# Optimization experiments

Measured on AMD Instinct MI355X. Metric: run time of the kernel, lower is better.

The kernel has to match this reference:

```python
import jax, jax.numpy as jnp
import numpy as np

HEADS = 16

def setup_inputs() -> dict:
    key = jax.random.key(0)
    k1, k2, k3 = jax.random.split(key, 3)
    B, S, D = 2, 2048, 1024
    return {
        "query": jax.random.normal(k1, (B, S, D), dtype=jnp.float32),
        "key": jax.random.normal(k2, (B, S, D), dtype=jnp.float32),
        "value": jax.random.normal(k3, (B, S, D), dtype=jnp.float32),
    }

def reference(query, key, value):
    B, S, D = query.shape
    H = HEADS
    dh = D // H
    # split(-1) into H equal chunks == reshape to (B, S, H, dh)
    q = query.reshape(B, S, H, dh)
    k = key.reshape(B, S, H, dh)
    v = value.reshape(B, S, H, dh)
    scale = 1.0 / jnp.sqrt(jnp.asarray(dh, dtype=query.dtype))
    scores = jnp.einsum('bqhd,bkhd->bhqk', q, k) * scale  # [B,H,S,S]
    probs = jax.nn.softmax(scores, axis=-1)
    out = jnp.einsum('bhqk,bkhd->bqhd', probs, v)  # [B,S,H,dh]
    return out.reshape(B, S, D)
```

## Files before the change

kernel.cpp:

```cpp
#include <hip/hip_runtime.h>
#include <stdint.h>


#define B_ 2
#define S_ 2048
#define D_ 1024
#define H_ 16
#define DH 64
#define M_TILE 128
#define N_TILE 128
#define NITER (S_ / N_TILE)

typedef __bf16 bf16;
typedef __bf16 bf16x2 __attribute__((ext_vector_type(2)));
typedef __bf16 bf16x4 __attribute__((ext_vector_type(4)));
typedef __bf16 bf16x8 __attribute__((ext_vector_type(8)));
typedef float floatx4 __attribute__((ext_vector_type(4)));

#define KB_HEAD (S_ * DH * 2)
#define KB_TOTAL (B_ * H_ * KB_HEAD)
#define VT_ROW (S_ * 2)
#define WS_NEEDED (2u * KB_TOTAL)

#define KTILE_B 16384
#define BUF_B 32768
#define LSH_OFF 65536
#define SMEM_MAIN (LSH_OFF + 512)
#define O_STRIDE 36

__device__ __forceinline__ float fast_exp2(float x) {
#if __has_builtin(__builtin_amdgcn_exp2f)
  return __builtin_amdgcn_exp2f(x);
#else
  return exp2f(x);
#endif
}

__device__ __forceinline__ void gl_lds16(const void* g, void* l) {
  __builtin_amdgcn_global_load_lds(
      (const __attribute__((address_space(1))) unsigned int*)g,
      (__attribute__((address_space(3))) unsigned int*)l, 16, 0, 0);
}

__global__ __launch_bounds__(256)
void prep(const float* __restrict__ Kg, const float* __restrict__ Vg,
          unsigned char* __restrict__ ws) {
  const int bid = blockIdx.x;
  const int tid = threadIdx.x;
  if (bid < 512) {
    __shared__ __align__(16) bf16 VTsh[64][132];
    const int head_lin = bid & 31, ktile = bid >> 5;
    const int b = head_lin >> 4, h = head_lin & 15;
    const int kb = ktile * 128;
    const int vr0 = (tid >> 3) << 2;
    const int vf0 = (tid & 7) << 3;
    const float* Vbase = Vg + (size_t)(b * S_) * D_ + h * DH;
    float vals[4][8];
#pragma unroll
    for (int rr = 0; rr < 4; ++rr) {
      const float* vp = Vbase + (size_t)(kb + vr0 + rr) * D_ + vf0;
      float4 a = *(const float4*)vp;
      float4 c = *(const float4*)(vp + 4);
      vals[rr][0] = a.x; vals[rr][1] = a.y; vals[rr][2] = a.z; vals[rr][3] = a.w;
      vals[rr][4] = c.x; vals[rr][5] = c.y; vals[rr][6] = c.z; vals[rr][7] = c.w;
    }
    const int pbase = (vr0 & 96) + ((vr0 >> 2) & 3) * 8 + ((vr0 >> 4) & 1) * 4;
#pragma unroll
    for (int j = 0; j < 8; ++j) {
      bf16x4 y = {(bf16)vals[0][j], (bf16)vals[1][j], (bf16)vals[2][j], (bf16)vals[3][j]};
      *(bf16x4*)(&VTsh[vf0 + j][pbase]) = y;
    }
    __syncthreads();
    const int f = tid >> 2, part = tid & 3;
    unsigned char* dst = ws + KB_TOTAL + (size_t)(head_lin * 64 + f) * VT_ROW + kb * 2 + part * 64;
#pragma unroll
    for (int c16 = 0; c16 < 4; ++c16) {
      bf16x8 v = *(const bf16x8*)(&VTsh[f][part * 32 + c16 * 8]);
      *(bf16x8*)(dst + c16 * 16) = v;
    }
  } else {
    const int cb = bid - 512;
#pragma unroll
    for (int i = 0; i < 8; ++i) {
      int idx = cb * 2048 + i * 256 + tid;
      int f4 = idx & 15;
      int hh = (idx >> 4) & 15;
      int s  = (idx >> 8) & 2047;
      int bb = idx >> 19;
      float4 x = *(const float4*)(Kg + (size_t)idx * 4);
      bf16x4 y = {(bf16)x.x, (bf16)x.y, (bf16)x.z, (bf16)x.w};
      *(bf16x4*)(ws + (size_t)(((bb * 16 + hh) * 2048 + s) * 16 + f4) * 8) = y;
    }
  }
}

__global__ __launch_bounds__(512, 4)
void attn_fwd(const float* __restrict__ Qg, const unsigned char* __restrict__ Kb,
              const unsigned char* __restrict__ VT, float* __restrict__ Og) {
  __shared__ __align__(16) unsigned char smem[SMEM_MAIN];
  float* Osh = (float*)smem;
  float* Lsh = (float*)(smem + LSH_OFF);

  const int tid  = threadIdx.x;
  const int lane = tid & 63;
  const int wave = tid >> 6;
  const int kw   = wave & 1;
  const int qw   = wave >> 1;
  const int col  = lane & 15;
  const int quad = lane >> 4;

  const int bid      = blockIdx.x;
  const int head_lin = bid & 31;
  const int qtile    = bid >> 5;
  const int b        = head_lin >> 4;
  const int h        = head_lin & 15;

  const unsigned char* Khead = Kb + (size_t)head_lin * KB_HEAD;
  const unsigned char* Vhead = VT + (size_t)head_lin * (DH * VT_ROW);

  const float QSCALE = 0.125f * 1.44269504088896340736f;

  bf16x8 Qf[2][2];
#pragma unroll
  for (int qt = 0; qt < 2; ++qt) {
    const float* base = Qg + (size_t)(b * S_ + qtile * M_TILE + qw * 32 + qt * 16 + col) * D_
                        + h * DH + quad * 8;
#pragma unroll
    for (int ks = 0; ks < 2; ++ks) {
      float4 x0 = *(const float4*)(base + ks * 32);
      float4 x1 = *(const float4*)(base + ks * 32 + 4);
      bf16x8 f;
      f[0] = (bf16)(x0.x * QSCALE); f[1] = (bf16)(x0.y * QSCALE);
      f[2] = (bf16)(x0.z * QSCALE); f[3] = (bf16)(x0.w * QSCALE);
      f[4] = (bf16)(x1.x * QSCALE); f[5] = (bf16)(x1.y * QSCALE);
      f[6] = (bf16)(x1.z * QSCALE); f[7] = (bf16)(x1.w * QSCALE);
      Qf[qt][ks] = f;
    }
  }

  floatx4 accO[4][2];
  float l_lane[2] = {0.f, 0.f};
#pragma unroll
  for (int ft = 0; ft < 4; ++ft)
#pragma unroll
    for (int qt = 0; qt < 2; ++qt) accO[ft][qt] = (floatx4)0.f;

  const int krow_b = wave * 16 + (lane >> 3);
  const int kcg    = lane & 7;
  const int vf_b   = wave * 8 + (lane >> 4);
  const int vcg    = lane & 15;

  const int krow0   = kw * 64 + col;
  const int ka0_off = krow0 * 128 + ((quad ^ (col & 7)) << 4);
  const int ka1_off = krow0 * 128 + (((quad | 4) ^ (col & 7)) << 4);
  const int va_c0   = KTILE_B + col * 256 + ((((kw << 3) | quad) ^ col) << 4);
  const int va_c1   = KTILE_B + col * 256 + ((((kw << 3) | 4 | quad) ^ col) << 4);

  auto dma_tile = [&](int kbk, int bufoff) {
#pragma unroll
    for (int t = 0; t < 2; ++t) {
      const int r = krow_b + t * 8;
      gl_lds16(Khead + (size_t)(kbk + r) * 128 + ((kcg ^ (r & 7)) << 4),
               smem + bufoff + (wave * 16 + t * 8) * 128);
    }
#pragma unroll
    for (int t = 0; t < 2; ++t) {
      const int f = vf_b + t * 4;
      gl_lds16(Vhead + (size_t)f * VT_ROW + kbk * 2 + ((vcg ^ (f & 15)) << 4),
               smem + bufoff + KTILE_B + (wave * 8 + t * 4) * 256);
    }
  };

  dma_tile(0, 0);
  __syncthreads();

  for (int it = 0; it < NITER; ++it) {
    const int bc = (it & 1) << 15;
    if (it + 1 < NITER) dma_tile((it + 1) * N_TILE, bc ^ BUF_B);

    floatx4 accS[4][2];
#pragma unroll
    for (int kt = 0; kt < 4; ++kt) {
      bf16x8 Ka0 = *(const bf16x8*)(smem + bc + ka0_off + kt * 2048);
      bf16x8 Ka1 = *(const bf16x8*)(smem + bc + ka1_off + kt * 2048);
#pragma unroll
      for (int qt = 0; qt < 2; ++qt) {
        floatx4 a = (floatx4)0.f;
        a = __builtin_amdgcn_mfma_f32_16x16x32_bf16(Ka0, Qf[qt][0], a, 0, 0, 0);
        a = __builtin_amdgcn_mfma_f32_16x16x32_bf16(Ka1, Qf[qt][1], a, 0, 0, 0);
        accS[kt][qt] = a;
      }
    }

#pragma unroll
    for (int qt = 0; qt < 2; ++qt) {
      float rs = 0.f;
#pragma unroll
      for (int kt = 0; kt < 4; ++kt)
#pragma unroll
        for (int r = 0; r < 4; ++r) {
          float p = fast_exp2(accS[kt][qt][r]);
          accS[kt][qt][r] = p;
          rs += p;
        }
      l_lane[qt] += rs;
    }

#pragma unroll
    for (int c = 0; c < 2; ++c) {
      bf16x8 Pf[2];
#pragma unroll
      for (int qt = 0; qt < 2; ++qt) {
        floatx4 p0 = accS[2 * c][qt], p1 = accS[2 * c + 1][qt];
        bf16x8 f = {(bf16)p0[0], (bf16)p0[1], (bf16)p0[2], (bf16)p0[3],
                    (bf16)p1[0], (bf16)p1[1], (bf16)p1[2], (bf16)p1[3]};
        Pf[qt] = f;
      }
      const int vo = c ? va_c1 : va_c0;
#pragma unroll
      for (int ft = 0; ft < 4; ++ft) {
        bf16x8 Va = *(const bf16x8*)(smem + bc + vo + ft * 4096);
#pragma unroll
        for (int qt = 0; qt < 2; ++qt)
          accO[ft][qt] = __builtin_amdgcn_mfma_f32_16x16x32_bf16(Va, Pf[qt], accO[ft][qt], 0, 0, 0);
      }
    }
    __syncthreads();
  }

  float l_red[2];
#pragma unroll
  for (int qt = 0; qt < 2; ++qt) {
    float s = l_lane[qt];
    s += __shfl_xor(s, 16);
    s += __shfl_xor(s, 32);
    l_red[qt] = s;
  }

  if (kw == 1) {
    float* r = Osh + (qw * 64 + lane) * O_STRIDE;
#pragma unroll
    for (int qt = 0; qt < 2; ++qt)
#pragma unroll
      for (int ft = 0; ft < 4; ++ft)
        *(floatx4*)(r + (qt * 4 + ft) * 4) = accO[ft][qt];
    if (quad == 0) {
#pragma unroll
      for (int qt = 0; qt < 2; ++qt)
        Lsh[qw * 32 + qt * 16 + col] = l_red[qt];
    }
  }
  __syncthreads();

  if (kw == 0) {
    const float* r = Osh + (qw * 64 + lane) * O_STRIDE;
    float rl[2];
#pragma unroll
    for (int qt = 0; qt < 2; ++qt)
      rl[qt] = 1.0f / (l_red[qt] + Lsh[qw * 32 + qt * 16 + col]);
#pragma unroll
    for (int qt = 0; qt < 2; ++qt) {
      const int q = qtile * M_TILE + qw * 32 + qt * 16 + col;
      float* dst = Og + (size_t)(b * S_ + q) * D_ + h * DH + quad * 4;
#pragma unroll
      for (int ft = 0; ft < 4; ++ft) {
        floatx4 o = (accO[ft][qt] + *(const floatx4*)(r + (qt * 4 + ft) * 4)) * rl[qt];
        *(floatx4*)(dst + ft * 16) = o;
      }
    }
  }
}

#define FB_K_STRIDE 68
#define FB_V_STRIDE 132
#define FB_K_BYTES (128 * FB_K_STRIDE * 2)
#define FB_V_BYTES (64 * FB_V_STRIDE * 2)
#define FB_ML_OFF (FB_K_BYTES + FB_V_BYTES)
#define FB_SMEM (FB_ML_OFF + 2048)

__device__ __forceinline__ bf16x8 cat8(bf16x4 a, bf16x4 b) {
  return __builtin_shufflevector(a, b, 0, 1, 2, 3, 4, 5, 6, 7);
}

__global__ __launch_bounds__(512, 4)
void attn_fwd_fb(const float* __restrict__ Qg, const float* __restrict__ Kg,
                 const float* __restrict__ Vg, float* __restrict__ Og) {
  __shared__ __align__(16) unsigned char smem[FB_SMEM > (256 * O_STRIDE * 4 + 2048) ? FB_SMEM : (256 * O_STRIDE * 4 + 2048)];
  bf16*  Ksh = (bf16*)smem;
  bf16*  Vsh = (bf16*)(smem + FB_K_BYTES);
  float* Osh = (float*)smem;
  float* Lsh = (float*)(smem + 256 * O_STRIDE * 4);

  const int tid  = threadIdx.x;
  const int lane = tid & 63;
  const int wave = tid >> 6;
  const int kw   = wave & 1;
  const int qw   = wave >> 1;
  const int col  = lane & 15;
  const int quad = lane >> 4;
  const int bid      = blockIdx.x;
  const int head_lin = bid & 31;
  const int qtile    = bid >> 5;
  const int b        = head_lin >> 4;
  const int h        = head_lin & 15;
  const float QSCALE = 0.125f * 1.44269504088896340736f;

  bf16x8 Qf[2][2];
#pragma unroll
  for (int qt = 0; qt < 2; ++qt) {
    const float* base = Qg + (size_t)(b * S_ + qtile * M_TILE + qw * 32 + qt * 16 + col) * D_
                        + h * DH + quad * 8;
#pragma unroll
    for (int ks = 0; ks < 2; ++ks) {
      float4 x0 = *(const float4*)(base + ks * 32);
      float4 x1 = *(const float4*)(base + ks * 32 + 4);
      bf16x8 f;
      f[0] = (bf16)(x0.x * QSCALE); f[1] = (bf16)(x0.y * QSCALE);
      f[2] = (bf16)(x0.z * QSCALE); f[3] = (bf16)(x0.w * QSCALE);
      f[4] = (bf16)(x1.x * QSCALE); f[5] = (bf16)(x1.y * QSCALE);
      f[6] = (bf16)(x1.z * QSCALE); f[7] = (bf16)(x1.w * QSCALE);
      Qf[qt][ks] = f;
    }
  }

  floatx4 accO[4][2];
  float l_lane[2] = {0.f, 0.f};
#pragma unroll
  for (int ft = 0; ft < 4; ++ft)
#pragma unroll
    for (int qt = 0; qt < 2; ++qt) accO[ft][qt] = (floatx4)0.f;

  const float* Kbase = Kg + (size_t)(b * S_) * D_ + h * DH;
  const float* Vbase = Vg + (size_t)(b * S_) * D_ + h * DH;
  const int krow0 = tid >> 4;
  const int kf4   = tid & 15;
  const int vk0   = (tid >> 3) * 2;
  const int vf0   = (tid & 7) * 8;

  for (int it = 0; it < NITER; ++it) {
    const int kb = it * N_TILE;
    float4 kx[4];
#pragma unroll
    for (int i = 0; i < 4; ++i)
      kx[i] = *(const float4*)(Kbase + (size_t)(kb + krow0 + 32 * i) * D_ + kf4 * 4);
    float4 va0 = *(const float4*)(Vbase + (size_t)(kb + vk0) * D_ + vf0);
    float4 va1 = *(const float4*)(Vbase + (size_t)(kb + vk0) * D_ + vf0 + 4);
    float4 vb0 = *(const float4*)(Vbase + (size_t)(kb + vk0 + 1) * D_ + vf0);
    float4 vb1 = *(const float4*)(Vbase + (size_t)(kb + vk0 + 1) * D_ + vf0 + 4);
#pragma unroll
    for (int i = 0; i < 4; ++i) {
      bf16x4 y = {(bf16)kx[i].x, (bf16)kx[i].y, (bf16)kx[i].z, (bf16)kx[i].w};
      *(bf16x4*)(Ksh + (krow0 + 32 * i) * FB_K_STRIDE + kf4 * 4) = y;
    }
    {
      float a[8] = {va0.x, va0.y, va0.z, va0.w, va1.x, va1.y, va1.z, va1.w};
      float c[8] = {vb0.x, vb0.y, vb0.z, vb0.w, vb1.x, vb1.y, vb1.z, vb1.w};
#pragma unroll
      for (int j = 0; j < 8; ++j) {
        bf16x2 y = {(bf16)a[j], (bf16)c[j]};
        *(bf16x2*)(Vsh + (vf0 + j) * FB_V_STRIDE + vk0) = y;
      }
    }
    __syncthreads();

    floatx4 accS[4][2];
#pragma unroll
    for (int kt = 0; kt < 4; ++kt) {
      const bf16* kp = Ksh + (kw * 64 + kt * 16 + col) * FB_K_STRIDE + quad * 8;
      bf16x8 Ka0 = cat8(*(const bf16x4*)kp, *(const bf16x4*)(kp + 4));
      bf16x8 Ka1 = cat8(*(const bf16x4*)(kp + 32), *(const bf16x4*)(kp + 36));
#pragma unroll
      for (int qt = 0; qt < 2; ++qt) {
        floatx4 a = (floatx4)0.f;
        a = __builtin_amdgcn_mfma_f32_16x16x32_bf16(Ka0, Qf[qt][0], a, 0, 0, 0);
        a = __builtin_amdgcn_mfma_f32_16x16x32_bf16(Ka1, Qf[qt][1], a, 0, 0, 0);
        accS[kt][qt] = a;
      }
    }
#pragma unroll
    for (int qt = 0; qt < 2; ++qt) {
      float rs = 0.f;
#pragma unroll
      for (int kt = 0; kt < 4; ++kt)
#pragma unroll
        for (int r = 0; r < 4; ++r) {
          float p = fast_exp2(accS[kt][qt][r]);
          accS[kt][qt][r] = p;
          rs += p;
        }
      l_lane[qt] += rs;
    }
#pragma unroll
    for (int c = 0; c < 2; ++c) {
      bf16x8 Pf[2];
#pragma unroll
      for (int qt = 0; qt < 2; ++qt) {
        floatx4 p0 = accS[2 * c][qt], p1 = accS[2 * c + 1][qt];
        bf16x8 f = {(bf16)p0[0], (bf16)p0[1], (bf16)p0[2], (bf16)p0[3],
                    (bf16)p1[0], (bf16)p1[1], (bf16)p1[2], (bf16)p1[3]};
        Pf[qt] = f;
      }
#pragma unroll
      for (int ft = 0; ft < 4; ++ft) {
        const bf16* vp = Vsh + (ft * 16 + col) * FB_V_STRIDE + kw * 64 + 32 * c + quad * 4;
        bf16x8 Va = cat8(*(const bf16x4*)vp, *(const bf16x4*)(vp + 16));
#pragma unroll
        for (int qt = 0; qt < 2; ++qt)
          accO[ft][qt] = __builtin_amdgcn_mfma_f32_16x16x32_bf16(Va, Pf[qt], accO[ft][qt], 0, 0, 0);
      }
    }
    __syncthreads();
  }

  float l_red[2];
#pragma unroll
  for (int qt = 0; qt < 2; ++qt) {
    float s = l_lane[qt];
    s += __shfl_xor(s, 16);
    s += __shfl_xor(s, 32);
    l_red[qt] = s;
  }
  if (kw == 1) {
    float* r = Osh + (qw * 64 + lane) * O_STRIDE;
#pragma unroll
    for (int qt = 0; qt < 2; ++qt)
#pragma unroll
      for (int ft = 0; ft < 4; ++ft)
        *(floatx4*)(r + (qt * 4 + ft) * 4) = accO[ft][qt];
    if (quad == 0) {
#pragma unroll
      for (int qt = 0; qt < 2; ++qt)
        Lsh[qw * 32 + qt * 16 + col] = l_red[qt];
    }
  }
  __syncthreads();
  if (kw == 0) {
    const float* r = Osh + (qw * 64 + lane) * O_STRIDE;
    float rl[2];
#pragma unroll
    for (int qt = 0; qt < 2; ++qt)
      rl[qt] = 1.0f / (l_red[qt] + Lsh[qw * 32 + qt * 16 + col]);
#pragma unroll
    for (int qt = 0; qt < 2; ++qt) {
      const int q = qtile * M_TILE + qw * 32 + qt * 16 + col;
      float* dst = Og + (size_t)(b * S_ + q) * D_ + h * DH + quad * 4;
#pragma unroll
      for (int ft = 0; ft < 4; ++ft) {
        floatx4 o = (accO[ft][qt] + *(const floatx4*)(r + (qt * 4 + ft) * 4)) * rl[qt];
        *(floatx4*)(dst + ft * 16) = o;
      }
    }
  }
}

extern "C" void kernel_launch(void* const* d_in, const int* in_sizes, int n_in,
                              void* d_out, int out_size, void* d_ws, size_t ws_size,
                              hipStream_t stream) {
  const float* Q = (const float*)d_in[0];
  const float* K = (const float*)d_in[1];
  const float* V = (const float*)d_in[2];
  float* O = (float*)d_out;
  if (ws_size >= WS_NEEDED && d_ws != nullptr) {
    unsigned char* ws = (unsigned char*)d_ws;
    hipLaunchKernelGGL(prep, dim3(1024), dim3(256), 0, stream, K, V, ws);
    hipLaunchKernelGGL(attn_fwd, dim3(B_ * H_ * (S_ / M_TILE)), dim3(512), 0, stream,
                       Q, ws, ws + KB_TOTAL, O);
  } else {
    hipLaunchKernelGGL(attn_fwd_fb, dim3(B_ * H_ * (S_ / M_TILE)), dim3(512), 0, stream,
                       Q, K, V, O);
  }
}
```

Baseline: 129.9 us.

## Halve attention tiles to 64x64, stagger KV start per block, vectorize K prep

Cuts the main attention kernel's query and key tiles from 128 to 64 and its block size from 512 to 256 threads, doubling the grid to 1024 blocks, and shrinks the shared-memory buffers so more blocks can reside per CU. Each block now begins its key/value sweep at an offset set by its query tile, so concurrent blocks read different KV tiles instead of all hitting the same one. The K conversion in prep is rewritten to use 8-wide bf16 stores in a head-major order and runs more blocks. The fallback kernel is changed to keep its 128 tiling. In exchange, K/V tiles are reused across fewer queries, so total KV traffic from L2 doubles and per-block sync overhead grows.

```diff
diff --git a/kernel.cpp b/kernel.cpp
--- a/kernel.cpp
+++ b/kernel.cpp
@@ -7,8 +7,8 @@
 #define D_ 1024
 #define H_ 16
 #define DH 64
-#define M_TILE 128
-#define N_TILE 128
+#define M_TILE 64
+#define N_TILE 64
 #define NITER (S_ / N_TILE)
 
 typedef __bf16 bf16;
@@ -22,9 +22,9 @@
 #define VT_ROW (S_ * 2)
 #define WS_NEEDED (2u * KB_TOTAL)
 
-#define KTILE_B 16384
-#define BUF_B 32768
-#define LSH_OFF 65536
+#define KTILE_B 8192
+#define BUF_B 16384
+#define LSH_OFF 32768
 #define SMEM_MAIN (LSH_OFF + 512)
 #define O_STRIDE 36
 
@@ -81,20 +81,23 @@
   } else {
     const int cb = bid - 512;
 #pragma unroll
-    for (int i = 0; i < 8; ++i) {
-      int idx = cb * 2048 + i * 256 + tid;
-      int f4 = idx & 15;
-      int hh = (idx >> 4) & 15;
-      int s  = (idx >> 8) & 2047;
-      int bb = idx >> 19;
-      float4 x = *(const float4*)(Kg + (size_t)idx * 4);
-      bf16x4 y = {(bf16)x.x, (bf16)x.y, (bf16)x.z, (bf16)x.w};
-      *(bf16x4*)(ws + (size_t)(((bb * 16 + hh) * 2048 + s) * 16 + f4) * 8) = y;
-    }
-  }
-}
-
-__global__ __launch_bounds__(512, 4)
+    for (int i = 0; i < 2; ++i) {
+      int idx = cb * 512 + i * 256 + tid;
+      int f8 = idx & 7;
+      int s  = (idx >> 3) & 2047;
+      int hh = (idx >> 14) & 15;
+      int bb = idx >> 18;
+      const float* src = Kg + (size_t)(bb * 2048 + s) * 1024 + hh * 64 + f8 * 8;
+      float4 x0 = ((const float4*)src)[0];
+      float4 x1 = ((const float4*)src)[1];
+      bf16x8 y = {(bf16)x0.x, (bf16)x0.y, (bf16)x0.z, (bf16)x0.w,
+                  (bf16)x1.x, (bf16)x1.y, (bf16)x1.z, (bf16)x1.w};
+      *(bf16x8*)(ws + (size_t)idx * 16) = y;
+    }
+  }
+}
+
+__global__ __launch_bounds__(256, 4)
 void attn_fwd(const float* __restrict__ Qg, const unsigned char* __restrict__ Kb,
               const unsigned char* __restrict__ VT, float* __restrict__ Og) {
   __shared__ __align__(16) unsigned char smem[SMEM_MAIN];
@@ -145,42 +148,40 @@
 #pragma unroll
     for (int qt = 0; qt < 2; ++qt) accO[ft][qt] = (floatx4)0.f;
 
-  const int krow_b = wave * 16 + (lane >> 3);
-  const int kcg    = lane & 7;
-  const int vf_b   = wave * 8 + (lane >> 4);
-  const int vcg    = lane & 15;
-
-  const int krow0   = kw * 64 + col;
-  const int ka0_off = krow0 * 128 + ((quad ^ (col & 7)) << 4);
-  const int ka1_off = krow0 * 128 + (((quad | 4) ^ (col & 7)) << 4);
-  const int va_c0   = KTILE_B + col * 256 + ((((kw << 3) | quad) ^ col) << 4);
-  const int va_c1   = KTILE_B + col * 256 + ((((kw << 3) | 4 | quad) ^ col) << 4);
+  const int dr = lane >> 3;
+  const int dc = (lane & 7) ^ dr;
+  const int c7      = col & 7;
+  const int ka0_off = (kw * 32 + col) * 128 + ((quad ^ c7) << 4);
+  const int ka1_off = (kw * 32 + col) * 128 + (((quad | 4) ^ c7) << 4);
+  const int va_off  = KTILE_B + col * 128 + ((((kw << 2) | quad) ^ c7) << 4);
 
   auto dma_tile = [&](int kbk, int bufoff) {
 #pragma unroll
-    for (int t = 0; t < 2; ++t) {
-      const int r = krow_b + t * 8;
-      gl_lds16(Khead + (size_t)(kbk + r) * 128 + ((kcg ^ (r & 7)) << 4),
-               smem + bufoff + (wave * 16 + t * 8) * 128);
-    }
-#pragma unroll
-    for (int t = 0; t < 2; ++t) {
-      const int f = vf_b + t * 4;
-      gl_lds16(Vhead + (size_t)f * VT_ROW + kbk * 2 + ((vcg ^ (f & 15)) << 4),
-               smem + bufoff + KTILE_B + (wave * 8 + t * 4) * 256);
+    for (int j = 0; j < 2; ++j) {
+      const int rf = wave * 16 + j * 8 + dr;
+      gl_lds16(Khead + (size_t)(kbk + rf) * 128 + (dc << 4),
+               smem + bufoff + (wave * 16 + j * 8) * 128);
+    }
+#pragma unroll
+    for (int j = 0; j < 2; ++j) {
+      const int rf = wave * 16 + j * 8 + dr;
+      gl_lds16(Vhead + (size_t)rf * VT_ROW + kbk * 2 + (dc << 4),
+               smem + bufoff + KTILE_B + (wave * 16 + j * 8) * 128);
     }
   };
 
-  dma_tile(0, 0);
+  const int start = qtile;
+  dma_tile((start & (NITER - 1)) * N_TILE, 0);
   __syncthreads();
 
   for (int it = 0; it < NITER; ++it) {
-    const int bc = (it & 1) << 15;
-    if (it + 1 < NITER) dma_tile((it + 1) * N_TILE, bc ^ BUF_B);
-
-    floatx4 accS[4][2];
-#pragma unroll
-    for (int kt = 0; kt < 4; ++kt) {
+    const int bc = (it & 1) << 14;
+    if (it + 1 < NITER)
+      dma_tile(((start + it + 1) & (NITER - 1)) * N_TILE, bc ^ BUF_B);
+
+    floatx4 accS[2][2];
+#pragma unroll
+    for (int kt = 0; kt < 2; ++kt) {
       bf16x8 Ka0 = *(const bf16x8*)(smem + bc + ka0_off + kt * 2048);
       bf16x8 Ka1 = *(const bf16x8*)(smem + bc + ka1_off + kt * 2048);
 #pragma unroll
@@ -196,7 +197,7 @@
     for (int qt = 0; qt < 2; ++qt) {
       float rs = 0.f;
 #pragma unroll
-      for (int kt = 0; kt < 4; ++kt)
+      for (int kt = 0; kt < 2; ++kt)
 #pragma unroll
         for (int r = 0; r < 4; ++r) {
           float p = fast_exp2(accS[kt][qt][r]);
@@ -206,24 +207,20 @@
       l_lane[qt] += rs;
     }
 
-#pragma unroll
-    for (int c = 0; c < 2; ++c) {
-      bf16x8 Pf[2];
-#pragma unroll
-      for (int qt = 0; qt < 2; ++qt) {
-        floatx4 p0 = accS[2 * c][qt], p1 = accS[2 * c + 1][qt];
-        bf16x8 f = {(bf16)p0[0], (bf16)p0[1], (bf16)p0[2], (bf16)p0[3],
-                    (bf16)p1[0], (bf16)p1[1], (bf16)p1[2], (bf16)p1[3]};
-        Pf[qt] = f;
-      }
-      const int vo = c ? va_c1 : va_c0;
-#pragma unroll
-      for (int ft = 0; ft < 4; ++ft) {
-        bf16x8 Va = *(const bf16x8*)(smem + bc + vo + ft * 4096);
-#pragma unroll
-        for (int qt = 0; qt < 2; ++qt)
-          accO[ft][qt] = __builtin_amdgcn_mfma_f32_16x16x32_bf16(Va, Pf[qt], accO[ft][qt], 0, 0, 0);
-      }
+    bf16x8 Pf[2];
+#pragma unroll
+    for (int qt = 0; qt < 2; ++qt) {
+      floatx4 p0 = accS[0][qt], p1 = accS[1][qt];
+      bf16x8 f = {(bf16)p0[0], (bf16)p0[1], (bf16)p0[2], (bf16)p0[3],
+                  (bf16)p1[0], (bf16)p1[1], (bf16)p1[2], (bf16)p1[3]};
+      Pf[qt] = f;
+    }
+#pragma unroll
+    for (int ft = 0; ft < 4; ++ft) {
+      bf16x8 Va = *(const bf16x8*)(smem + bc + va_off + ft * 2048);
+#pragma unroll
+      for (int qt = 0; qt < 2; ++qt)
+        accO[ft][qt] = __builtin_amdgcn_mfma_f32_16x16x32_bf16(Va, Pf[qt], accO[ft][qt], 0, 0, 0);
     }
     __syncthreads();
   }
@@ -271,12 +268,12 @@
   }
 }
 
+#define FB_NITER 16
 #define FB_K_STRIDE 68
 #define FB_V_STRIDE 132
 #define FB_K_BYTES (128 * FB_K_STRIDE * 2)
 #define FB_V_BYTES (64 * FB_V_STRIDE * 2)
-#define FB_ML_OFF (FB_K_BYTES + FB_V_BYTES)
-#define FB_SMEM (FB_ML_OFF + 2048)
+#define FB_SMEM ((256 * O_STRIDE * 4 + 2048) > (FB_K_BYTES + FB_V_BYTES) ? (256 * O_STRIDE * 4 + 2048) : (FB_K_BYTES + FB_V_BYTES))
 
 __device__ __forceinline__ bf16x8 cat8(bf16x4 a, bf16x4 b) {
   return __builtin_shufflevector(a, b, 0, 1, 2, 3, 4, 5, 6, 7);
@@ -285,7 +282,7 @@
 __global__ __launch_bounds__(512, 4)
 void attn_fwd_fb(const float* __restrict__ Qg, const float* __restrict__ Kg,
                  const float* __restrict__ Vg, float* __restrict__ Og) {
-  __shared__ __align__(16) unsigned char smem[FB_SMEM > (256 * O_STRIDE * 4 + 2048) ? FB_SMEM : (256 * O_STRIDE * 4 + 2048)];
+  __shared__ __align__(16) unsigned char smem[FB_SMEM];
   bf16*  Ksh = (bf16*)smem;
   bf16*  Vsh = (bf16*)(smem + FB_K_BYTES);
   float* Osh = (float*)smem;
@@ -308,7 +305,7 @@
   bf16x8 Qf[2][2];
 #pragma unroll
   for (int qt = 0; qt < 2; ++qt) {
-    const float* base = Qg + (size_t)(b * S_ + qtile * M_TILE + qw * 32 + qt * 16 + col) * D_
+    const float* base = Qg + (size_t)(b * S_ + qtile * 128 + qw * 32 + qt * 16 + col) * D_
                         + h * DH + quad * 8;
 #pragma unroll
     for (int ks = 0; ks < 2; ++ks) {
@@ -337,8 +334,8 @@
   const int vk0   = (tid >> 3) * 2;
   const int vf0   = (tid & 7) * 8;
 
-  for (int it = 0; it < NITER; ++it) {
-    const int kb = it * N_TILE;
+  for (int it = 0; it < FB_NITER; ++it) {
+    const int kb = it * 128;
     float4 kx[4];
 #pragma unroll
     for (int i = 0; i < 4; ++i)
@@ -442,7 +439,7 @@
       rl[qt] = 1.0f / (l_red[qt] + Lsh[qw * 32 + qt * 16 + col]);
 #pragma unroll
     for (int qt = 0; qt < 2; ++qt) {
-      const int q = qtile * M_TILE + qw * 32 + qt * 16 + col;
+      const int q = qtile * 128 + qw * 32 + qt * 16 + col;
       float* dst = Og + (size_t)(b * S_ + q) * D_ + h * DH + quad * 4;
 #pragma unroll
       for (int ft = 0; ft < 4; ++ft) {
@@ -462,11 +459,10 @@
   float* O = (float*)d_out;
   if (ws_size >= WS_NEEDED && d_ws != nullptr) {
     unsigned char* ws = (unsigned char*)d_ws;
-    hipLaunchKernelGGL(prep, dim3(1024), dim3(256), 0, stream, K, V, ws);
-    hipLaunchKernelGGL(attn_fwd, dim3(B_ * H_ * (S_ / M_TILE)), dim3(512), 0, stream,
+    hipLaunchKernelGGL(prep, dim3(1536), dim3(256), 0, stream, K, V, ws);
+    hipLaunchKernelGGL(attn_fwd, dim3(B_ * H_ * (S_ / M_TILE)), dim3(256), 0, stream,
                        Q, ws, ws + KB_TOTAL, O);
   } else {
-    hipLaunchKernelGGL(attn_fwd_fb, dim3(B_ * H_ * (S_ / M_TILE)), dim3(512), 0, stream,
-                       Q, K, V, O);
-  }
-}
+    hipLaunchKernelGGL(attn_fwd_fb, dim3(512), dim3(512), 0, stream, Q, K, V, O);
+  }
+}
```

New measurement: 134.6 us. 1.04x slower.
